# Kernel tuning notes

Hardware: AMD Instinct MI355X
Metric: run time of the kernel (lower is better)

## Reference

```python
import jax, jax.numpy as jnp
import numpy as np

N_NODES = 100000


def gcn_layer(x, edge_index, W, b):
    # GCNConv: out = D^{-1/2} (A + I) D^{-1/2} (x W) + b
    N = x.shape[0]
    loop = jnp.arange(N, dtype=edge_index.dtype)
    src = jnp.concatenate([edge_index[0], loop])
    dst = jnp.concatenate([edge_index[1], loop])
    deg = jax.ops.segment_sum(jnp.ones_like(src, dtype=x.dtype), dst, num_segments=N)
    dinv = jnp.where(deg > 0, jax.lax.rsqrt(deg), 0.0)
    norm = dinv[src] * dinv[dst]  # [E+N]
    h = x @ W  # [N, out]
    msg = h[src] * norm[:, None]  # [E+N, out]
    out = jax.ops.segment_sum(msg, dst, num_segments=N)
    return out + b


def setup_inputs() -> dict:
    key = jax.random.key(0)
    ks = jax.random.split(key, 8)
    x = jax.random.normal(ks[0], (N_NODES, 128), dtype=jnp.float32)
    edge_index = jax.random.randint(ks[1], (2, 1600000), 0, N_NODES, dtype=jnp.int32)
    def glorot(k, fan_in, fan_out):
        s = jnp.sqrt(6.0 / (fan_in + fan_out)).astype(jnp.float32)
        return jax.random.uniform(k, (fan_in, fan_out), jnp.float32, -s, s)
    return {
        "x": x,
        "edge_index": edge_index,
        "W1": glorot(ks[2], 128, 64), "b1": jnp.zeros((64,), jnp.float32),
        "W2": glorot(ks[3], 64, 128), "b2": jnp.zeros((128,), jnp.float32),
        "W3": glorot(ks[4], 128, 64), "b3": jnp.zeros((64,), jnp.float32),
    }


def reference(x, edge_index, W1, b1, W2, b2, W3, b3):
    h = jax.nn.relu(gcn_layer(x, edge_index, W1, b1))
    h = jax.nn.relu(gcn_layer(h, edge_index, W2, b2))
    out = gcn_layer(h, edge_index, W3, b3)
    return out
```

## Files before the change

kernel.cpp:

```cpp
#include <hip/hip_runtime.h>
#include <hip/hip_fp16.h>
#include <stdint.h>


#define NWGA 256
#define CMAX 8

typedef _Float16 half8 __attribute__((ext_vector_type(8)));
typedef float f32x4 __attribute__((ext_vector_type(4)));

struct __align__(8) Half4 { __half x, y, z, w; };

__global__ __launch_bounds__(256) void bucket_hist_kernel(
    const int* __restrict__ dst, int E, int chunk, int NBUK,
    int* __restrict__ M ) {
  __shared__ int hist[512];
  const int w = blockIdx.x, t = threadIdx.x;
  for (int i = t; i < NBUK; i += 256) hist[i] = 0;
  __syncthreads();
  const int e0 = w * chunk;
  const int e1 = min(e0 + chunk, E);
  for (int e = e0 + t; e < e1; e += 256) atomicAdd(&hist[dst[e] >> 8], 1);
  __syncthreads();
  for (int i = t; i < NBUK; i += 256) M[i * NWGA + w] = hist[i];
}

__global__ void scan_blocksum(const int* __restrict__ data, int len,
                              int* __restrict__ bsum) {
  __shared__ int s[256];
  int i = blockIdx.x * 256 + threadIdx.x;
  s[threadIdx.x] = (i < len) ? data[i] : 0;
  __syncthreads();
  for (int off = 128; off > 0; off >>= 1) {
    if (threadIdx.x < off) s[threadIdx.x] += s[threadIdx.x + off];
    __syncthreads();
  }
  if (threadIdx.x == 0) bsum[blockIdx.x] = s[0];
}

__global__ void scan_bsums(int* bsum, int NB) {
  __shared__ int s[512];
  int t = threadIdx.x;
  int v = (t < NB) ? bsum[t] : 0;
  s[t] = v;
  __syncthreads();
  for (int off = 1; off < 512; off <<= 1) {
    int u = (t >= off) ? s[t - off] : 0;
    __syncthreads();
    s[t] += u;
    __syncthreads();
  }
  if (t < NB) bsum[t] = s[t] - v;
}

__global__ void scan_final(int* __restrict__ data, int len,
                           const int* __restrict__ bsum) {
  __shared__ int s[256];
  int t = threadIdx.x;
  int i = blockIdx.x * 256 + t;
  int v = (i < len) ? data[i] : 0;
  s[t] = v;
  __syncthreads();
  for (int off = 1; off < 256; off <<= 1) {
    int u = (t >= off) ? s[t - off] : 0;
    __syncthreads();
    s[t] += u;
    __syncthreads();
  }
  if (i < len) data[i] = bsum[blockIdx.x] + s[t] - v;
}

__global__ __launch_bounds__(256) void bucket_scatter_kernel(
    const int* __restrict__ ei, int E, int chunk, int NBUK,
    const int* __restrict__ Mscan, int2* __restrict__ edata1) {
  __shared__ int cur[512];
  const int w = blockIdx.x, t = threadIdx.x;
  for (int i = t; i < NBUK; i += 256) cur[i] = Mscan[i * NWGA + w];
  __syncthreads();
  const int e0 = w * chunk;
  const int e1 = min(e0 + chunk, E);
  for (int e = e0 + t; e < e1; e += 256) {
    int s = ei[e];
    int d = ei[E + e];
    int pos = atomicAdd(&cur[d >> 8], 1);
    edata1[pos] = make_int2(s, d);
  }
}

__global__ __launch_bounds__(256) void bucket_sort_kernel(
    const int2* __restrict__ edata1, const int* __restrict__ Mscan, int E,
    int N, int NBUK, int* __restrict__ offsets, float* __restrict__ dinv,
    int* __restrict__ edata2) {
  __shared__ int hist[256];
  __shared__ int cursor[256];
  const int b = blockIdx.x, t = threadIdx.x;
  const int ebase = Mscan[b * NWGA];
  const int eend = (b + 1 < NBUK) ? Mscan[(b + 1) * NWGA] : E;
  const int nodebase = b << 8;
  const int node = nodebase + t;
  const int base = ebase + min(nodebase, N);
  hist[t] = (node < N) ? 1 : 0;
  __syncthreads();
  for (int e = ebase + t; e < eend; e += 256)
    atomicAdd(&hist[edata1[e].y - nodebase], 1);
  __syncthreads();
  const int deg = hist[t];
  for (int off = 1; off < 256; off <<= 1) {
    int u = (t >= off) ? hist[t - off] : 0;
    __syncthreads();
    hist[t] += u;
    __syncthreads();
  }
  const int excl = hist[t] - deg;
  cursor[t] = base + excl + 1;
  if (node < N) {
    offsets[node] = base + excl;
    dinv[node] = rsqrtf((float)deg);
    edata2[base + excl] = node;
  }
  if (node == N - 1) offsets[N] = E + N;
  __syncthreads();
  for (int e = ebase + t; e < eend; e += 256) {
    int2 sd = edata1[e];
    int pos = atomicAdd(&cursor[sd.y - nodebase], 1);
    edata2[pos] = sd.x;
  }
}

__global__ __launch_bounds__(256) void edge_weight_kernel(
    const int* __restrict__ edata2, int EN, int* __restrict__ ed3) {
  int stride = gridDim.x * blockDim.x;
  for (int e = blockIdx.x * blockDim.x + threadIdx.x; e < EN; e += stride)
    ed3[e] = edata2[e] << 7;
}

template <int K, int D, bool BR, bool DSCALE, typename InT>
__global__ __launch_bounds__(256) void gemm_mfma(
    const InT* __restrict__ X, const float* __restrict__ W,
    const float* __restrict__ bias, const float* __restrict__ dinv,
    _Float16* __restrict__ H, int N) {
  __shared__ char lds[2 * K * D];
  const int t = threadIdx.x;
  for (int idx = t; idx < K * D; idx += 256) {
    const int k = idx % K;
    const int d = idx / K;
    const _Float16 v = (_Float16)W[k * D + d];
    const int byte =
        d * (2 * K) + ((((k >> 3) ^ (d & 7)) << 4) | ((k & 7) << 1));
    *(_Float16*)(lds + byte) = v;
  }
  __syncthreads();

  const int w = t >> 6;
  const int l = t & 63;
  const int lrow = l & 15;
  const int lg = l >> 4;
  const int r0 = blockIdx.x * 128 + w * 32;
  if (r0 >= N) return;

  f32x4 acc[2][D / 16];
#pragma unroll
  for (int rt = 0; rt < 2; ++rt)
#pragma unroll
    for (int c = 0; c < D / 16; ++c) acc[rt][c] = (f32x4){0.f, 0.f, 0.f, 0.f};

  int rA[2];
  rA[0] = min(r0 + lrow, N - 1);
  rA[1] = min(r0 + 16 + lrow, N - 1);

#pragma unroll
  for (int s = 0; s < K / 32; ++s) {
    half8 a[2];
#pragma unroll
    for (int rt = 0; rt < 2; ++rt) {
      if constexpr (sizeof(InT) == 2) {
        a[rt] = *reinterpret_cast<const half8*>(
            (const _Float16*)X + (size_t)rA[rt] * K + s * 32 + lg * 8);
      } else {
        const float* xp = (const float*)X + (size_t)rA[rt] * K + s * 32 + lg * 8;
        float4 lo = *reinterpret_cast<const float4*>(xp);
        float4 hi = *reinterpret_cast<const float4*>(xp + 4);
        half8 af;
        af[0] = (_Float16)lo.x; af[1] = (_Float16)lo.y;
        af[2] = (_Float16)lo.z; af[3] = (_Float16)lo.w;
        af[4] = (_Float16)hi.x; af[5] = (_Float16)hi.y;
        af[6] = (_Float16)hi.z; af[7] = (_Float16)hi.w;
        a[rt] = af;
      }
    }
    half8 b[D / 16];
#pragma unroll
    for (int c = 0; c < D / 16; ++c) {
      const int d = c * 16 + lrow;
      const int g = s * 4 + lg;
      b[c] = *reinterpret_cast<const half8*>(
          lds + d * (2 * K) + (((g ^ (d & 7)) << 4)));
    }
#pragma unroll
    for (int rt = 0; rt < 2; ++rt)
#pragma unroll
      for (int c = 0; c < D / 16; ++c)
        acc[rt][c] = __builtin_amdgcn_mfma_f32_16x16x32_f16(a[rt], b[c],
                                                            acc[rt][c], 0, 0, 0);
  }

  float bv[D / 16];
  if (BR) {
#pragma unroll
    for (int c = 0; c < D / 16; ++c) bv[c] = bias[c * 16 + lrow];
  }
#pragma unroll
  for (int rt = 0; rt < 2; ++rt) {
#pragma unroll
    for (int r = 0; r < 4; ++r) {
      const int row = r0 + rt * 16 + lg * 4 + r;
      if (row < N) {
        float ds = 1.f;
        if (DSCALE) ds = dinv[row];
#pragma unroll
        for (int c = 0; c < D / 16; ++c) {
          float v = acc[rt][c][r];
          if (BR) v = fmaxf(v + bv[c], 0.f);
          if (DSCALE) v *= ds;
          H[(size_t)row * D + c * 16 + lrow] = (_Float16)v;
        }
      }
    }
  }
}

template <bool BIAS, bool RELU, bool SCALE_OUT, typename OutT>
__global__ __launch_bounds__(256) void agg_kernel(
    const __half* __restrict__ h, const int* __restrict__ ed,
    const int* __restrict__ offsets, const float* __restrict__ dinv,
    const float* __restrict__ bias, OutT* __restrict__ out, int N) {
  const int wid = blockIdx.x * 4 + (threadIdx.x >> 6);
  const int na = wid * 8;
  if (na >= N) return;
  const int lane = threadIdx.x & 63;
  const int nrem = min(8, N - na);

  const int off_l = offsets[na + min(lane, nrem)];
  const float dn_l = dinv[na + min(lane, nrem - 1)];
  const int eb0 = __shfl(off_l, 0);
  const int eb1 = __shfl(off_l, nrem);
  float bsv = 0.f;
  if (BIAS) bsv = bias[lane];

  int pe[CMAX];
#pragma unroll
  for (int c = 0; c < CMAX; ++c) {
    int idx = eb0 + c * 64 + lane;
    pe[c] = ed[min(idx, eb1 - 1)];
  }

  const char* hb = (const char*)h;
  float acc = 0.f;
  int cur = 0;
  int bnd = __shfl(off_l, 1);
  float dn = __shfl(dn_l, 0);
  int j = eb0;

#define FLUSH()                                                        \
  {                                                                    \
    float v = acc * dn;                                                \
    if (BIAS) v += bsv;                                                \
    if (RELU) v = fmaxf(v, 0.f);                                       \
    if (SCALE_OUT) v *= dn;                                            \
    if constexpr (sizeof(OutT) == 2)                                   \
      out[(size_t)(na + cur) * 64 + lane] = __float2half(v);           \
    else                                                               \
      out[(size_t)(na + cur) * 64 + lane] = v;                         \
    acc = 0.f;                                                         \
    cur++;                                                             \
    bnd = __shfl(off_l, min(cur + 1, 8));                              \
    dn = __shfl(dn_l, min(cur, 7));                                    \
  }

#pragma unroll
  for (int c = 0; c < CMAX; ++c) {
    if (j < eb1) {
      const int pc = pe[c];
      for (int k = 0; k < 64; k += 8) {
        if (j >= eb1) break;
        int so[8];
        float g[8], wv[8];
#pragma unroll
        for (int i = 0; i < 8; ++i) {
          so[i] = __shfl(pc, k + i);
          wv[i] = (j + i < eb1) ? 1.f : 0.f;
        }
#pragma unroll
        for (int i = 0; i < 8; ++i)
          g[i] = __half2float(
              *(const __half*)(hb + (size_t)(unsigned)so[i] + lane * 2));
#pragma unroll
        for (int i = 0; i < 8; ++i) {
          if (j + i == bnd) FLUSH();
          acc = fmaf(g[i], wv[i], acc);
        }
        j += 8;
      }
    }
  }
  for (; j < eb1; ++j) {
    int so = ed[j];
    float g =
        __half2float(*(const __half*)(hb + (size_t)(unsigned)so + lane * 2));
    if (j == bnd) FLUSH();
    acc += g;
  }
  if (cur < nrem) FLUSH();
#undef FLUSH
}

extern "C" void kernel_launch(void* const* d_in, const int* in_sizes, int n_in,
                              void* d_out, int out_size, void* d_ws,
                              size_t ws_size, hipStream_t stream) {
  const float* x  = (const float*)d_in[0];
  const int*   ei = (const int*)d_in[1];
  const float* W1 = (const float*)d_in[2];
  const float* b1 = (const float*)d_in[3];
  const float* W2 = (const float*)d_in[4];
  const float* b2 = (const float*)d_in[5];
  const float* W3 = (const float*)d_in[6];
  const float* b3 = (const float*)d_in[7];

  const int N = in_sizes[0] / 128;
  const int E = in_sizes[1] / 2;
  const int EN = E + N;
  const int NBUK = (N + 255) >> 8;
  const int MLEN = NBUK * NWGA;
  const int chunk = (E + NWGA - 1) / NWGA;

  char* w = (char*)d_ws;
  int* offsets = (int*)w;      w += (size_t)(N + 2) * 4;
  float* dinv = (float*)w;     w += (size_t)N * 4;
  w = (char*)(((uintptr_t)w + 255) & ~(uintptr_t)255);
  int* edata3 = (int*)w;       w += (size_t)EN * 4;
  w = (char*)(((uintptr_t)w + 255) & ~(uintptr_t)255);
  char* regionA = w;           w += (size_t)N * 64 * 2;
  w = (char*)(((uintptr_t)w + 255) & ~(uintptr_t)255);
  char* regionB = w;           w += (size_t)E * 8;
  w = (char*)(((uintptr_t)w + 255) & ~(uintptr_t)255);
  char* regionC = w;           w += (size_t)N * 128 * 2;

  int* M = (int*)regionA;
  int* bsum = M + MLEN;
  int* edata2 = bsum + 512;
  _Float16* ht1 = (_Float16*)regionA;
  int2* edata1 = (int2*)regionB;
  _Float16* a2 = (_Float16*)regionB;
  _Float16* hout1 = (_Float16*)regionC;
  _Float16* h2 = (_Float16*)regionC;

  const int NBS = (MLEN + 255) / 256;
  const int NW = (N + 7) / 8;
  const int AGB = (NW + 3) / 4;
  const int GGB = (N + 127) / 128;

  bucket_hist_kernel<<<NWGA, 256, 0, stream>>>(ei + E, E, chunk, NBUK, M);
  scan_blocksum<<<NBS, 256, 0, stream>>>(M, MLEN, bsum);
  scan_bsums<<<1, 512, 0, stream>>>(bsum, NBS);
  scan_final<<<NBS, 256, 0, stream>>>(M, MLEN, bsum);
  bucket_scatter_kernel<<<NWGA, 256, 0, stream>>>(ei, E, chunk, NBUK, M, edata1);
  bucket_sort_kernel<<<NBUK, 256, 0, stream>>>(edata1, M, E, N, NBUK, offsets,
                                               dinv, edata2);
  edge_weight_kernel<<<1024, 256, 0, stream>>>(edata2, EN, edata3);

  gemm_mfma<128, 64, false, true, float><<<GGB, 256, 0, stream>>>(
      x, W1, nullptr, dinv, ht1, N);
  agg_kernel<true, true, true, __half><<<AGB, 256, 0, stream>>>(
      (const __half*)ht1, edata3, offsets, dinv, b1, (__half*)hout1, N);

  agg_kernel<false, false, false, __half><<<AGB, 256, 0, stream>>>(
      (const __half*)hout1, edata3, offsets, dinv, nullptr, (__half*)a2, N);
  gemm_mfma<64, 128, true, false, _Float16><<<GGB, 256, 0, stream>>>(
      a2, W2, b2, nullptr, h2, N);

  gemm_mfma<128, 64, false, true, _Float16><<<GGB, 256, 0, stream>>>(
      h2, W3, nullptr, dinv, ht1, N);
  agg_kernel<true, false, false, float><<<AGB, 256, 0, stream>>>(
      (const __half*)ht1, edata3, offsets, dinv, b3, (float*)d_out, N);
}
```

Before: 337.7 us.

## Pad CSR rows to even length and gather two edges per wavefront with half2 loads

```diff
diff --git a/kernel.cpp b/kernel.cpp
--- a/kernel.cpp
+++ b/kernel.cpp
@@ -87,51 +87,93 @@
   }
 }
 
-__global__ __launch_bounds__(256) void bucket_sort_kernel(
+__global__ __launch_bounds__(256) void bucket_deg_kernel(
     const int2* __restrict__ edata1, const int* __restrict__ Mscan, int E,
-    int N, int NBUK, int* __restrict__ offsets, float* __restrict__ dinv,
-    int* __restrict__ edata2) {
+    int N, int NBUK, int* __restrict__ deg_arr, float* __restrict__ dinv,
+    int* __restrict__ bsum2) {
   __shared__ int hist[256];
+  __shared__ int red[256];
+  const int b = blockIdx.x, t = threadIdx.x;
+  const int ebase = Mscan[b * NWGA];
+  const int eend = (b + 1 < NBUK) ? Mscan[(b + 1) * NWGA] : E;
+  const int nodebase = b << 8;
+  const int node = nodebase + t;
+  hist[t] = 0;
+  __syncthreads();
+  for (int e = ebase + t; e < eend; e += 256)
+    atomicAdd(&hist[edata1[e].y - nodebase], 1);
+  __syncthreads();
+  int pd = 0;
+  if (node < N) {
+    int dt = hist[t] + 1;
+    pd = dt + (dt & 1);
+    deg_arr[node] = dt;
+    dinv[node] = rsqrtf((float)dt);
+  }
+  red[t] = pd;
+  __syncthreads();
+  for (int off = 128; off > 0; off >>= 1) {
+    if (t < off) red[t] += red[t + off];
+    __syncthreads();
+  }
+  if (t == 0) bsum2[b] = red[0];
+}
+
+__global__ void bucket_base_scan(int* bsum2, int NBUK, int* offsets, int N) {
+  __shared__ int s[512];
+  int t = threadIdx.x;
+  int v = (t < NBUK) ? bsum2[t] : 0;
+  s[t] = v;
+  __syncthreads();
+  for (int off = 1; off < 512; off <<= 1) {
+    int u = (t >= off) ? s[t - off] : 0;
+    __syncthreads();
+    s[t] += u;
+    __syncthreads();
+  }
+  if (t < NBUK) bsum2[t] = s[t] - v;
+  if (t == NBUK - 1) offsets[N] = s[t];
+}
+
+__global__ __launch_bounds__(256) void bucket_fill_kernel(
+    const int2* __restrict__ edata1, const int* __restrict__ Mscan,
+    const int* __restrict__ deg_arr, const int* __restrict__ bsum2, int E,
+    int N, int NBUK, int* __restrict__ offsets, int* __restrict__ ed3) {
+  __shared__ int scan[256];
   __shared__ int cursor[256];
   const int b = blockIdx.x, t = threadIdx.x;
   const int ebase = Mscan[b * NWGA];
   const int eend = (b + 1 < NBUK) ? Mscan[(b + 1) * NWGA] : E;
   const int nodebase = b << 8;
   const int node = nodebase + t;
-  const int base = ebase + min(nodebase, N);
-  hist[t] = (node < N) ? 1 : 0;
-  __syncthreads();
-  for (int e = ebase + t; e < eend; e += 256)
-    atomicAdd(&hist[edata1[e].y - nodebase], 1);
-  __syncthreads();
-  const int deg = hist[t];
+  const int dt = (node < N) ? deg_arr[node] : 0;
+  const int pd = dt + (dt & 1);
+  scan[t] = pd;
+  __syncthreads();
   for (int off = 1; off < 256; off <<= 1) {
-    int u = (t >= off) ? hist[t - off] : 0;
-    __syncthreads();
-    hist[t] += u;
-    __syncthreads();
-  }
-  const int excl = hist[t] - deg;
-  cursor[t] = base + excl + 1;
+    int u = (t >= off) ? scan[t - off] : 0;
+    __syncthreads();
+    scan[t] += u;
+    __syncthreads();
+  }
+  const int base = bsum2[b] + scan[t] - pd;
+  cursor[t] = base + 1;
   if (node < N) {
-    offsets[node] = base + excl;
-    dinv[node] = rsqrtf((float)deg);
-    edata2[base + excl] = node;
-  }
-  if (node == N - 1) offsets[N] = E + N;
+    offsets[node] = base;
+    ed3[base] = node << 7;
+    if (dt & 1) ed3[base + dt] = N << 7;
+  }
   __syncthreads();
   for (int e = ebase + t; e < eend; e += 256) {
     int2 sd = edata1[e];
     int pos = atomicAdd(&cursor[sd.y - nodebase], 1);
-    edata2[pos] = sd.x;
-  }
-}
-
-__global__ __launch_bounds__(256) void edge_weight_kernel(
-    const int* __restrict__ edata2, int EN, int* __restrict__ ed3) {
-  int stride = gridDim.x * blockDim.x;
-  for (int e = blockIdx.x * blockDim.x + threadIdx.x; e < EN; e += stride)
-    ed3[e] = edata2[e] << 7;
+    ed3[pos] = sd.x << 7;
+  }
+}
+
+__global__ void zero_rows_kernel(_Float16* a, _Float16* b) {
+  if (threadIdx.x < 64) a[threadIdx.x] = (_Float16)0.f;
+  else b[threadIdx.x - 64] = (_Float16)0.f;
 }
 
 template <int K, int D, bool BR, bool DSCALE, typename InT>
@@ -238,14 +280,16 @@
   const int na = wid * 8;
   if (na >= N) return;
   const int lane = threadIdx.x & 63;
+  const int half32 = lane >> 5;
+  const int fpair = lane & 31;
   const int nrem = min(8, N - na);
 
   const int off_l = offsets[na + min(lane, nrem)];
   const float dn_l = dinv[na + min(lane, nrem - 1)];
   const int eb0 = __shfl(off_l, 0);
   const int eb1 = __shfl(off_l, nrem);
-  float bsv = 0.f;
-  if (BIAS) bsv = bias[lane];
+  float2 bsv = make_float2(0.f, 0.f);
+  if (BIAS) bsv = *reinterpret_cast<const float2*>(&bias[fpair * 2]);
 
   int pe[CMAX];
 #pragma unroll
@@ -254,64 +298,69 @@
     pe[c] = ed[min(idx, eb1 - 1)];
   }
 
-  const char* hb = (const char*)h;
-  float acc = 0.f;
+  const char* hb = (const char*)h + (fpair << 2);
+  float ax = 0.f, ay = 0.f;
   int cur = 0;
   int bnd = __shfl(off_l, 1);
   float dn = __shfl(dn_l, 0);
   int j = eb0;
 
-#define FLUSH()                                                        \
-  {                                                                    \
-    float v = acc * dn;                                                \
-    if (BIAS) v += bsv;                                                \
-    if (RELU) v = fmaxf(v, 0.f);                                       \
-    if (SCALE_OUT) v *= dn;                                            \
-    if constexpr (sizeof(OutT) == 2)                                   \
-      out[(size_t)(na + cur) * 64 + lane] = __float2half(v);           \
-    else                                                               \
-      out[(size_t)(na + cur) * 64 + lane] = v;                         \
-    acc = 0.f;                                                         \
-    cur++;                                                             \
-    bnd = __shfl(off_l, min(cur + 1, 8));                              \
-    dn = __shfl(dn_l, min(cur, 7));                                    \
-  }
+  auto flush = [&]() {
+    float tx = ax + __shfl_xor(ax, 32);
+    float ty = ay + __shfl_xor(ay, 32);
+    float vx = tx * dn, vy = ty * dn;
+    if (BIAS) { vx += bsv.x; vy += bsv.y; }
+    if (RELU) { vx = fmaxf(vx, 0.f); vy = fmaxf(vy, 0.f); }
+    if (SCALE_OUT) { vx *= dn; vy *= dn; }
+    if (lane < 32) {
+      if constexpr (sizeof(OutT) == 2) {
+        *reinterpret_cast<__half2*>((char*)out + ((size_t)(na + cur) << 7) +
+                                    (fpair << 2)) = __floats2half2_rn(vx, vy);
+      } else {
+        *reinterpret_cast<float2*>((char*)out + ((size_t)(na + cur) << 8) +
+                                   (fpair << 3)) = make_float2(vx, vy);
+      }
+    }
+    ax = 0.f; ay = 0.f;
+    cur++;
+    bnd = __shfl(off_l, min(cur + 1, 8));
+    dn = __shfl(dn_l, min(cur, 7));
+  };
 
 #pragma unroll
   for (int c = 0; c < CMAX; ++c) {
     if (j < eb1) {
       const int pc = pe[c];
-      for (int k = 0; k < 64; k += 8) {
+      for (int kp = 0; kp < 64; kp += 8) {
         if (j >= eb1) break;
-        int so[8];
-        float g[8], wv[8];
-#pragma unroll
-        for (int i = 0; i < 8; ++i) {
-          so[i] = __shfl(pc, k + i);
-          wv[i] = (j + i < eb1) ? 1.f : 0.f;
-        }
-#pragma unroll
-        for (int i = 0; i < 8; ++i)
-          g[i] = __half2float(
-              *(const __half*)(hb + (size_t)(unsigned)so[i] + lane * 2));
-#pragma unroll
-        for (int i = 0; i < 8; ++i) {
-          if (j + i == bnd) FLUSH();
-          acc = fmaf(g[i], wv[i], acc);
+        int so[4];
+        float2 g[4];
+#pragma unroll
+        for (int i = 0; i < 4; ++i)
+          so[i] = __shfl(pc, kp + 2 * i + half32);
+#pragma unroll
+        for (int i = 0; i < 4; ++i)
+          g[i] = __half22float2(*reinterpret_cast<const __half2*>(
+              hb + (size_t)(unsigned)so[i]));
+#pragma unroll
+        for (int i = 0; i < 4; ++i) {
+          if (j + 2 * i == bnd) flush();
+          ax += g[i].x;
+          ay += g[i].y;
         }
         j += 8;
       }
     }
   }
-  for (; j < eb1; ++j) {
-    int so = ed[j];
-    float g =
-        __half2float(*(const __half*)(hb + (size_t)(unsigned)so + lane * 2));
-    if (j == bnd) FLUSH();
-    acc += g;
-  }
-  if (cur < nrem) FLUSH();
-#undef FLUSH
+  for (; j < eb1; j += 2) {
+    int so = ed[j + half32];
+    float2 g = __half22float2(
+        *reinterpret_cast<const __half2*>(hb + (size_t)(unsigned)so));
+    if (j == bnd) flush();
+    ax += g.x;
+    ay += g.y;
+  }
+  if (cur < nrem) flush();
 }
 
 extern "C" void kernel_launch(void* const* d_in, const int* in_sizes, int n_in,
@@ -328,7 +377,6 @@
 
   const int N = in_sizes[0] / 128;
   const int E = in_sizes[1] / 2;
-  const int EN = E + N;
   const int NBUK = (N + 255) >> 8;
   const int MLEN = NBUK * NWGA;
   const int chunk = (E + NWGA - 1) / NWGA;
@@ -336,10 +384,12 @@
   char* w = (char*)d_ws;
   int* offsets = (int*)w;      w += (size_t)(N + 2) * 4;
   float* dinv = (float*)w;     w += (size_t)N * 4;
+  int* deg_arr = (int*)w;      w += (size_t)N * 4;
+  int* bsum2 = (int*)w;        w += 512 * 4;
   w = (char*)(((uintptr_t)w + 255) & ~(uintptr_t)255);
-  int* edata3 = (int*)w;       w += (size_t)EN * 4;
+  int* edata3 = (int*)w;       w += (size_t)(E + 2 * N) * 4;
   w = (char*)(((uintptr_t)w + 255) & ~(uintptr_t)255);
-  char* regionA = w;           w += (size_t)N * 64 * 2;
+  char* regionA = w;           w += (size_t)(N + 1) * 64 * 2;
   w = (char*)(((uintptr_t)w + 255) & ~(uintptr_t)255);
   char* regionB = w;           w += (size_t)E * 8;
   w = (char*)(((uintptr_t)w + 255) & ~(uintptr_t)255);
@@ -347,7 +397,6 @@
 
   int* M = (int*)regionA;
   int* bsum = M + MLEN;
-  int* edata2 = bsum + 512;
   _Float16* ht1 = (_Float16*)regionA;
   int2* edata1 = (int2*)regionB;
   _Float16* a2 = (_Float16*)regionB;
@@ -359,14 +408,18 @@
   const int AGB = (NW + 3) / 4;
   const int GGB = (N + 127) / 128;
 
+  zero_rows_kernel<<<1, 128, 0, stream>>>(ht1 + (size_t)N * 64,
+                                          hout1 + (size_t)N * 64);
   bucket_hist_kernel<<<NWGA, 256, 0, stream>>>(ei + E, E, chunk, NBUK, M);
   scan_blocksum<<<NBS, 256, 0, stream>>>(M, MLEN, bsum);
   scan_bsums<<<1, 512, 0, stream>>>(bsum, NBS);
   scan_final<<<NBS, 256, 0, stream>>>(M, MLEN, bsum);
   bucket_scatter_kernel<<<NWGA, 256, 0, stream>>>(ei, E, chunk, NBUK, M, edata1);
-  bucket_sort_kernel<<<NBUK, 256, 0, stream>>>(edata1, M, E, N, NBUK, offsets,
-                                               dinv, edata2);
-  edge_weight_kernel<<<1024, 256, 0, stream>>>(edata2, EN, edata3);
+  bucket_deg_kernel<<<NBUK, 256, 0, stream>>>(edata1, M, E, N, NBUK, deg_arr,
+                                              dinv, bsum2);
+  bucket_base_scan<<<1, 512, 0, stream>>>(bsum2, NBUK, offsets, N);
+  bucket_fill_kernel<<<NBUK, 256, 0, stream>>>(edata1, M, deg_arr, bsum2, E, N,
+                                               NBUK, offsets, edata3);
 
   gemm_mfma<128, 64, false, true, float><<<GGB, 256, 0, stream>>>(
       x, W1, nullptr, dinv, ht1, N);
```

New measurement: 323.4 us. 1.04x faster.
